# Optimization experiments

Hardware: AMD Instinct MI355X
Metric: run time of the kernel (lower is better)

The kernel has to match this reference:

```python
import jax, jax.numpy as jnp
import numpy as np

D_MODEL, D_K, D_V, H = 1024, 64, 64, 16
B, N = 4, 2048


def setup_inputs() -> dict:
    key = jax.random.key(0)
    ks = jax.random.split(key, 11)
    s = 0.02
    return {
        "Q": jax.random.normal(ks[0], (B, N, D_MODEL), jnp.float32),
        "K": jax.random.normal(ks[1], (B, N, D_MODEL), jnp.float32),
        "V": jax.random.normal(ks[2], (B, N, D_MODEL), jnp.float32),
        # stacked per-head projection weights: [h, d_model, d_k]
        "Wq": jax.random.normal(ks[3], (H, D_MODEL, D_K), jnp.float32) * s,
        "bq": jax.random.normal(ks[4], (H, D_K), jnp.float32) * s,
        "Wk": jax.random.normal(ks[5], (H, D_MODEL, D_K), jnp.float32) * s,
        "bk": jax.random.normal(ks[6], (H, D_K), jnp.float32) * s,
        "Wv": jax.random.normal(ks[7], (H, D_MODEL, D_V), jnp.float32) * s,
        "bv": jax.random.normal(ks[8], (H, D_V), jnp.float32) * s,
        "Wo": jax.random.normal(ks[9], (H * D_V, D_MODEL), jnp.float32) * s,
        "bo": jax.random.normal(ks[10], (D_MODEL,), jnp.float32) * s,
        "apply_mask": 1,
    }


def reference(Q, K, V, Wq, bq, Wk, bk, Wv, bv, Wo, bo, apply_mask):
    # fused per-head projections: [b, h, n, d_k]
    q = jnp.einsum("bnd,hdk->bhnk", Q, Wq) + bq[None, :, None, :]
    k = jnp.einsum("bnd,hdk->bhnk", K, Wk) + bk[None, :, None, :]
    v = jnp.einsum("bnd,hdv->bhnv", V, Wv) + bv[None, :, None, :]
    scores = jnp.einsum("bhnk,bhmk->bhnm", q, k) / jnp.sqrt(
        jnp.asarray(D_K, q.dtype)
    )
    if apply_mask:
        n = Q.shape[1]
        causal = jnp.tril(jnp.ones((n, n), dtype=bool))
        scores = jnp.where(causal[None, None], scores, -jnp.inf)
    weights = jax.nn.softmax(scores, axis=-1)
    out = jnp.einsum("bhnm,bhmv->bhnv", weights, v)
    # concat heads: [b, n, h*d_v]
    out = out.transpose(0, 2, 1, 3).reshape(Q.shape[0], Q.shape[1], H * D_V)
    return out @ Wo + bo
```

## Files before the change

### kernel.cpp

```cpp
#include <hip/hip_runtime.h>
#include <hip/hip_bf16.h>

#define H 16
#define DM 1024
#define DK 64
#define B_ 4
#define N_ 2048

typedef __attribute__((ext_vector_type(8))) short bf16x8;
typedef __attribute__((ext_vector_type(4))) short s16x4;
typedef __attribute__((ext_vector_type(4))) float f32x4;

static __device__ __forceinline__ short f2bs(float x) {
    __hip_bfloat16 b = __float2bfloat16(x);
    return *reinterpret_cast<short*>(&b);
}

static __device__ __forceinline__ void async16(const void* g, void* l) {
    __builtin_amdgcn_global_load_lds(
        (const __attribute__((address_space(1))) void*)g,
        (__attribute__((address_space(3))) void*)l, 16, 0, 0);
}

__global__ __launch_bounds__(256) void prep_kernel(
    const float* __restrict__ Q, const float* __restrict__ K, const float* __restrict__ V,
    const float* __restrict__ Wq, const float* __restrict__ Wk,
    const float* __restrict__ Wv, const float* __restrict__ Wo,
    short* __restrict__ Qb, short* __restrict__ Kb, short* __restrict__ Vb,
    short* __restrict__ wqT, short* __restrict__ wkT,
    short* __restrict__ wvT, short* __restrict__ woT)
{
    int y = blockIdx.y;
    if (y < 3) {
        const float* s = (y == 0) ? Q : (y == 1) ? K : V;
        short* d = (y == 0) ? Qb : (y == 1) ? Kb : Vb;
        size_t i = ((size_t)blockIdx.x * 256 + threadIdx.x) * 8;
        f32x4 a = *(const f32x4*)(s + i);
        f32x4 b = *(const f32x4*)(s + i + 4);
        bf16x8 p;
        #pragma unroll
        for (int j = 0; j < 4; ++j) { p[j] = f2bs(a[j]); p[4 + j] = f2bs(b[j]); }
        *(bf16x8*)(d + i) = p;
        return;
    }
    if (blockIdx.x >= 1024) return;
    __shared__ float tile[64][65];
    int z = blockIdx.x >> 8;
    int bx = blockIdx.x & 255;
    int t = threadIdx.x;
    int tj = t & 63, ti = t >> 6;

    if (z < 3) {
        const float* src = (z == 0) ? Wq : (z == 1) ? Wk : Wv;
        short* dst = (z == 0) ? wqT : (z == 1) ? wkT : wvT;
        int h = bx >> 4;
        int dmt = bx & 15;
        #pragma unroll
        for (int r = 0; r < 16; ++r) {
            int i = r * 4 + ti;
            tile[i][tj] = src[((size_t)h * 1024 + dmt * 64 + i) * 64 + tj];
        }
        __syncthreads();
        #pragma unroll
        for (int r = 0; r < 16; ++r) {
            int dk = r * 4 + ti;
            dst[((size_t)h * 64 + dk) * 1024 + dmt * 64 + tj] = f2bs(tile[tj][dk]);
        }
    } else {
        int kt = bx >> 4;
        int nt = bx & 15;
        #pragma unroll
        for (int r = 0; r < 16; ++r) {
            int i = r * 4 + ti;
            tile[i][tj] = Wo[((size_t)kt * 64 + i) * 1024 + nt * 64 + tj];
        }
        __syncthreads();
        #pragma unroll
        for (int r = 0; r < 16; ++r) {
            int jn = r * 4 + ti;
            woT[((size_t)nt * 64 + jn) * 1024 + kt * 64 + tj] = f2bs(tile[tj][jn]);
        }
    }
}

static __device__ __forceinline__ void gemm_stage(
    const char* Ab, const char* Bb, size_t kb, char* As, char* Bs, int lane, int w)
{
    int r0 = w * 32 + (lane >> 2);
    int g  = ((lane & 3) ^ ((lane >> 3) & 3)) << 4;
    int dst0 = w * 2048 + lane * 16;
    async16(Ab + (size_t)r0 * 2048 + kb + g, As + dst0);
    async16(Ab + (size_t)(r0 + 16) * 2048 + kb + g, As + dst0 + 1024);
    async16(Bb + (size_t)r0 * 2048 + kb + g, Bs + dst0);
    async16(Bb + (size_t)(r0 + 16) * 2048 + kb + g, Bs + dst0 + 1024);
}

static __device__ __forceinline__ void gemm_mainloop(
    const short* __restrict__ A, const short* __restrict__ BT,
    int rowM0, int colN0, char* As, char* Bs, f32x4 (&acc)[4][4])
{
    int tid = threadIdx.x;
    int lane = tid & 63, w = tid >> 6;
    int l16 = lane & 15, quad = lane >> 4;
    int wm = w >> 1, wn = w & 1;
    int xg = (quad ^ ((l16 >> 1) & 3)) << 4;

    const char* Ab = (const char*)A + (size_t)rowM0 * 2048;
    const char* Bb = (const char*)BT + (size_t)colN0 * 2048;

    gemm_stage(Ab, Bb, 0, As, Bs, lane, w);
    for (int it = 0; it < 32; ++it) {
        __syncthreads();
        int cur = (it & 1) * 8192;
        if (it + 1 < 32) {
            int nxt = ((it + 1) & 1) * 8192;
            gemm_stage(Ab, Bb, (size_t)(it + 1) * 64, As + nxt, Bs + nxt, lane, w);
        }
        bf16x8 a[4], b[4];
        #pragma unroll
        for (int i = 0; i < 4; ++i)
            a[i] = *(const bf16x8*)(As + cur + (wm * 64 + i * 16 + l16) * 64 + xg);
        #pragma unroll
        for (int j = 0; j < 4; ++j)
            b[j] = *(const bf16x8*)(Bs + cur + (wn * 64 + j * 16 + l16) * 64 + xg);
        #pragma unroll
        for (int i = 0; i < 4; ++i)
            #pragma unroll
            for (int j = 0; j < 4; ++j)
                acc[i][j] = __builtin_amdgcn_mfma_f32_16x16x32_bf16(a[i], b[j], acc[i][j], 0, 0, 0);
    }
}

__global__ __launch_bounds__(256) void proj_gemm(
    const short* __restrict__ Qb, const short* __restrict__ Kb, const short* __restrict__ Vb,
    const short* __restrict__ wqT, const short* __restrict__ wkT, const short* __restrict__ wvT,
    const float* __restrict__ bq, const float* __restrict__ bk, const float* __restrict__ bv,
    short* __restrict__ qbuf, short* __restrict__ kbuf, short* __restrict__ vTbuf)
{
    __shared__ char As[16384], Bs[16384];
    int which = blockIdx.z;
    const short* A  = (which == 0) ? Qb : (which == 1) ? Kb : Vb;
    const short* BT = (which == 0) ? wqT : (which == 1) ? wkT : wvT;
    const float* bias = (which == 0) ? bq : (which == 1) ? bk : bv;

    int rowM0 = blockIdx.x * 128;
    int colN0 = blockIdx.y * 128;

    f32x4 acc[4][4];
    #pragma unroll
    for (int i = 0; i < 4; ++i)
        #pragma unroll
        for (int j = 0; j < 4; ++j) acc[i][j] = (f32x4){0.f, 0.f, 0.f, 0.f};

    gemm_mainloop(A, BT, rowM0, colN0, As, Bs, acc);

    int lane = threadIdx.x & 63, w = threadIdx.x >> 6;
    int l16 = lane & 15, quad = lane >> 4;
    int wm = w >> 1, wn = w & 1;

    if (which == 2) {
        #pragma unroll
        for (int j = 0; j < 4; ++j) {
            int col = colN0 + wn * 64 + j * 16 + l16;
            int hh = col >> 6, dv = col & 63;
            float bs = bias[col];
            #pragma unroll
            for (int i = 0; i < 4; ++i) {
                int rowb = rowM0 + wm * 64 + i * 16 + quad * 4;
                int bb = rowb >> 11, n0 = rowb & 2047;
                s16x4 pk;
                #pragma unroll
                for (int r = 0; r < 4; ++r) pk[r] = f2bs(acc[i][j][r] + bs);
                *(s16x4*)(vTbuf + (((size_t)bb * H + hh) * DK + dv) * N_ + n0) = pk;
            }
        }
    } else {
        short* dst = (which == 0) ? qbuf : kbuf;
        float scl = (which == 0) ? 0.180336880f : 1.0f;
        #pragma unroll
        for (int j = 0; j < 4; ++j) {
            int col = colN0 + wn * 64 + j * 16 + l16;
            float bs = bias[col];
            #pragma unroll
            for (int i = 0; i < 4; ++i) {
                int rowb = rowM0 + wm * 64 + i * 16 + quad * 4;
                #pragma unroll
                for (int r = 0; r < 4; ++r)
                    dst[(size_t)(rowb + r) * 1024 + col] = f2bs((acc[i][j][r] + bs) * scl);
            }
        }
    }
}

__global__ __launch_bounds__(256) void out_gemm(
    const short* __restrict__ obuf, const short* __restrict__ woT,
    const float* __restrict__ bo, float* __restrict__ out)
{
    __shared__ char As[16384], Bs[16384];
    int rowM0 = blockIdx.x * 128;
    int colN0 = blockIdx.y * 128;

    f32x4 acc[4][4];
    #pragma unroll
    for (int i = 0; i < 4; ++i)
        #pragma unroll
        for (int j = 0; j < 4; ++j) acc[i][j] = (f32x4){0.f, 0.f, 0.f, 0.f};

    gemm_mainloop(obuf, woT, rowM0, colN0, As, Bs, acc);

    int lane = threadIdx.x & 63, w = threadIdx.x >> 6;
    int l16 = lane & 15, quad = lane >> 4;
    int wm = w >> 1, wn = w & 1;

    #pragma unroll
    for (int j = 0; j < 4; ++j) {
        int col = colN0 + wn * 64 + j * 16 + l16;
        float bs = bo[col];
        #pragma unroll
        for (int i = 0; i < 4; ++i) {
            int rowb = rowM0 + wm * 64 + i * 16 + quad * 4;
            #pragma unroll
            for (int r = 0; r < 4; ++r)
                out[(size_t)(rowb + r) * 1024 + col] = acc[i][j][r] + bs;
        }
    }
}

__global__ __launch_bounds__(256) void flash_kernel(
    const short* __restrict__ qbuf, const short* __restrict__ kbuf, const short* __restrict__ vT,
    short* __restrict__ obuf, const int* __restrict__ amask)
{
    __shared__ short Ks[2][4096];
    __shared__ short Vs[2][4096];
    __shared__ char  plds[4][2048];

    int bid = blockIdx.x;
    int g = bid & 7, idx = bid >> 3;
    int bh = g * 8 + (idx >> 4);
    int xq = idx & 15;
    int b = bh >> 4, h = bh & 15;

    int tid = threadIdx.x;
    int lane = tid & 63, wave = tid >> 6;
    int l16 = lane & 15, quad = lane >> 4;
    int msk = amask[0];

    int i8 = lane >> 3, i7 = lane & 7;
    int sg = (i7 ^ i8) << 4;
    int pk0 = i8 * 4 + wave;
    int skey = wave * 16 + i8;
    int ldst = wave * 2048 + lane * 16;

    const char* kbase = (const char*)(kbuf + (size_t)b * 2048 * 1024 + h * 64);
    const char* vbase = (const char*)(vT + ((size_t)(b * 16 + h) * 64) * 2048);

    int m7 = l16 & 7;
    int g0 = (quad ^ m7) << 4;
    int g1 = ((4 | quad) ^ m7) << 4;

    char* pw = plds[wave];
    int prd0 = l16 * 128 + g0;
    int prd1 = l16 * 128 + g1;

    for (int pass = 0; pass < 2; ++pass) {
        int qt = pass ? (31 - xq) : xq;
        int qw = qt * 64 + wave * 16;
        int nkb = msk ? (qt + 1) : 32;

        const short* qp = qbuf + ((size_t)(b * 2048 + qw + l16)) * 1024 + h * 64;
        bf16x8 aq0 = *(const bf16x8*)(qp + quad * 8);
        bf16x8 aq1 = *(const bf16x8*)(qp + 32 + quad * 8);

        f32x4 o[4];
        float lsum[4];
        #pragma unroll
        for (int i = 0; i < 4; ++i) { o[i] = (f32x4){0.f, 0.f, 0.f, 0.f}; lsum[i] = 0.f; }

        async16(kbase + (size_t)pk0 * 2048 + sg, (char*)Ks[0] + ldst);
        async16(kbase + (size_t)(pk0 + 32) * 2048 + sg, (char*)Ks[0] + ldst + 1024);
        async16(vbase + (size_t)skey * 4096 + sg, (char*)Vs[0] + ldst);
        async16(vbase + (size_t)(skey + 8) * 4096 + sg, (char*)Vs[0] + ldst + 1024);

        for (int ib = 0; ib < nkb; ++ib) {
            __syncthreads();
            int cur = ib & 1;
            if (ib + 1 < nkb) {
                int nb = (ib + 1) & 1;
                size_t kb2 = (size_t)(ib + 1) * 64;
                async16(kbase + (kb2 + pk0) * 2048 + sg, (char*)Ks[nb] + ldst);
                async16(kbase + (kb2 + pk0 + 32) * 2048 + sg, (char*)Ks[nb] + ldst + 1024);
                async16(vbase + (size_t)skey * 4096 + kb2 * 2 + sg, (char*)Vs[nb] + ldst);
                async16(vbase + (size_t)(skey + 8) * 4096 + kb2 * 2 + sg, (char*)Vs[nb] + ldst + 1024);
            }
            int kb = ib * 64;

            f32x4 s[4];
            #pragma unroll
            for (int nt = 0; nt < 4; ++nt) {
                const char* kr = (const char*)Ks[cur] + (nt * 16 + l16) * 128;
                bf16x8 b0 = *(const bf16x8*)(kr + g0);
                bf16x8 b1 = *(const bf16x8*)(kr + g1);
                f32x4 t = (f32x4){0.f, 0.f, 0.f, 0.f};
                t = __builtin_amdgcn_mfma_f32_16x16x32_bf16(aq0, b0, t, 0, 0, 0);
                t = __builtin_amdgcn_mfma_f32_16x16x32_bf16(aq1, b1, t, 0, 0, 0);
                s[nt] = t;
            }

            if (msk && (kb + 63 > qw)) {
                #pragma unroll
                for (int r = 0; r < 4; ++r) {
                    int row = qw + quad * 4 + r;
                    #pragma unroll
                    for (int nt = 0; nt < 4; ++nt) {
                        int col = kb + l16 * 4 + nt;
                        if (col > row) s[nt][r] = -3e38f;
                    }
                }
            }

            #pragma unroll
            for (int r = 0; r < 4; ++r) {
                float p0 = exp2f(s[0][r]), p1 = exp2f(s[1][r]);
                float p2 = exp2f(s[2][r]), p3 = exp2f(s[3][r]);
                s[0][r] = p0; s[1][r] = p1; s[2][r] = p2; s[3][r] = p3;
                lsum[r] += (p0 + p1) + (p2 + p3);
            }

            __builtin_amdgcn_wave_barrier();
            #pragma unroll
            for (int r = 0; r < 4; ++r) {
                int row = quad * 4 + r;
                s16x4 pk;
                pk[0] = f2bs(s[0][r]); pk[1] = f2bs(s[1][r]);
                pk[2] = f2bs(s[2][r]); pk[3] = f2bs(s[3][r]);
                *(s16x4*)(pw + row * 128 + (((l16 >> 1) ^ (row & 7)) << 4) + ((l16 & 1) << 3)) = pk;
            }
            __builtin_amdgcn_wave_barrier();
            bf16x8 ap0 = *(const bf16x8*)(pw + prd0);
            bf16x8 ap1 = *(const bf16x8*)(pw + prd1);
            __builtin_amdgcn_wave_barrier();

            #pragma unroll
            for (int vb = 0; vb < 4; ++vb) {
                const char* vr = (const char*)Vs[cur] + (vb * 16 + l16) * 128;
                bf16x8 v0 = *(const bf16x8*)(vr + g0);
                bf16x8 v1 = *(const bf16x8*)(vr + g1);
                o[vb] = __builtin_amdgcn_mfma_f32_16x16x32_bf16(ap0, v0, o[vb], 0, 0, 0);
                o[vb] = __builtin_amdgcn_mfma_f32_16x16x32_bf16(ap1, v1, o[vb], 0, 0, 0);
            }
        }

        #pragma unroll
        for (int r = 0; r < 4; ++r) {
            float t = lsum[r];
            #pragma unroll
            for (int off = 1; off < 16; off <<= 1) t += __shfl_xor(t, off, 64);
            float inv = 1.0f / t;
            int row = qw + quad * 4 + r;
            #pragma unroll
            for (int vb = 0; vb < 4; ++vb)
                obuf[((size_t)(b * 2048 + row)) * 1024 + h * 64 + vb * 16 + l16] =
                    f2bs(o[vb][r] * inv);
        }
        __syncthreads();
    }
}

extern "C" void kernel_launch(void* const* d_in, const int* in_sizes, int n_in,
                              void* d_out, int out_size, void* d_ws, size_t ws_size,
                              hipStream_t stream)
{
    const float* Q  = (const float*)d_in[0];
    const float* K  = (const float*)d_in[1];
    const float* V  = (const float*)d_in[2];
    const float* Wq = (const float*)d_in[3];
    const float* bq = (const float*)d_in[4];
    const float* Wk = (const float*)d_in[5];
    const float* bk = (const float*)d_in[6];
    const float* Wv = (const float*)d_in[7];
    const float* bv = (const float*)d_in[8];
    const float* Wo = (const float*)d_in[9];
    const float* bo = (const float*)d_in[10];
    const int* amask = (const int*)d_in[11];
    float* out = (float*)d_out;

    char* ws = (char*)d_ws;
    const size_t SZ = (size_t)B_ * N_ * DM * sizeof(short);
    const size_t SZW = (size_t)H * DK * DM * sizeof(short);
    short* Qb    = (short*)ws; ws += SZ;
    short* Kb    = (short*)ws; ws += SZ;
    short* Vb    = (short*)ws; ws += SZ;
    short* qbuf  = (short*)ws; ws += SZ;
    short* kbuf  = (short*)ws; ws += SZ;
    short* vTbuf = (short*)ws; ws += SZ;
    short* wqT   = (short*)ws; ws += SZW;
    short* wkT   = (short*)ws; ws += SZW;
    short* wvT   = (short*)ws; ws += SZW;
    short* woT   = (short*)ws; ws += SZW;
    short* obuf  = Qb;

    prep_kernel<<<dim3(4096, 4), dim3(256), 0, stream>>>(Q, K, V, Wq, Wk, Wv, Wo,
                                                         Qb, Kb, Vb, wqT, wkT, wvT, woT);
    proj_gemm<<<dim3(64, 8, 3), dim3(256), 0, stream>>>(Qb, Kb, Vb, wqT, wkT, wvT,
                                                        bq, bk, bv, qbuf, kbuf, vTbuf);
    flash_kernel<<<dim3(1024), dim3(256), 0, stream>>>(qbuf, kbuf, vTbuf, obuf, amask);
    out_gemm<<<dim3(64, 8), dim3(256), 0, stream>>>(obuf, woT, bo, out);
}
```

Before: 358.1 us.

## Use register-staged GEMM loads, raw exp2, and truncating bf16 pack in attention

The GEMM mainloop swaps async global-to-LDS double buffering for loads into registers that are then stored to a single LDS buffer, which halves shared memory per block and adds a second barrier per iteration. In the attention kernel, exp2f becomes the hardware exp2 builtin and the P values are packed to bf16 with a byte permute (truncation rather than round-to-nearest). Swizzled write addresses are precomputed once. The aim is higher occupancy and fewer VALU instructions in the softmax, at the cost of slightly lower precision and less load/compute overlap in the GEMM.

```diff
diff --git a/kernel.cpp b/kernel.cpp
--- a/kernel.cpp
+++ b/kernel.cpp
@@ -9,6 +9,7 @@
 
 typedef __attribute__((ext_vector_type(8))) short bf16x8;
 typedef __attribute__((ext_vector_type(4))) short s16x4;
+typedef __attribute__((ext_vector_type(2))) unsigned int u32x2;
 typedef __attribute__((ext_vector_type(4))) float f32x4;
 
 static __device__ __forceinline__ short f2bs(float x) {
@@ -20,6 +21,10 @@
     __builtin_amdgcn_global_load_lds(
         (const __attribute__((address_space(1))) void*)g,
         (__attribute__((address_space(3))) void*)l, 16, 0, 0);
+}
+
+static __device__ __forceinline__ unsigned packbf(float lo, float hi) {
+    return __builtin_amdgcn_perm(__float_as_uint(hi), __float_as_uint(lo), 0x07060302u);
 }
 
 __global__ __launch_bounds__(256) void prep_kernel(
@@ -83,18 +88,6 @@
     }
 }
 
-static __device__ __forceinline__ void gemm_stage(
-    const char* Ab, const char* Bb, size_t kb, char* As, char* Bs, int lane, int w)
-{
-    int r0 = w * 32 + (lane >> 2);
-    int g  = ((lane & 3) ^ ((lane >> 3) & 3)) << 4;
-    int dst0 = w * 2048 + lane * 16;
-    async16(Ab + (size_t)r0 * 2048 + kb + g, As + dst0);
-    async16(Ab + (size_t)(r0 + 16) * 2048 + kb + g, As + dst0 + 1024);
-    async16(Bb + (size_t)r0 * 2048 + kb + g, Bs + dst0);
-    async16(Bb + (size_t)(r0 + 16) * 2048 + kb + g, Bs + dst0 + 1024);
-}
-
 static __device__ __forceinline__ void gemm_mainloop(
     const short* __restrict__ A, const short* __restrict__ BT,
     int rowM0, int colN0, char* As, char* Bs, f32x4 (&acc)[4][4])
@@ -105,24 +98,41 @@
     int wm = w >> 1, wn = w & 1;
     int xg = (quad ^ ((l16 >> 1) & 3)) << 4;
 
-    const char* Ab = (const char*)A + (size_t)rowM0 * 2048;
-    const char* Bb = (const char*)BT + (size_t)colN0 * 2048;
-
-    gemm_stage(Ab, Bb, 0, As, Bs, lane, w);
+    int r0 = w * 32 + (lane >> 2);
+    int gsl = ((lane & 3) ^ ((lane >> 3) & 3)) << 4;
+    int dst0 = w * 2048 + lane * 16;
+    const char* Ag0 = (const char*)A + (size_t)(rowM0 + r0) * 2048 + gsl;
+    const char* Ag1 = (const char*)A + (size_t)(rowM0 + r0 + 16) * 2048 + gsl;
+    const char* Bg0 = (const char*)BT + (size_t)(colN0 + r0) * 2048 + gsl;
+    const char* Bg1 = (const char*)BT + (size_t)(colN0 + r0 + 16) * 2048 + gsl;
+
+    bf16x8 ga0 = *(const bf16x8*)Ag0;
+    bf16x8 ga1 = *(const bf16x8*)Ag1;
+    bf16x8 gb0 = *(const bf16x8*)Bg0;
+    bf16x8 gb1 = *(const bf16x8*)Bg1;
+
     for (int it = 0; it < 32; ++it) {
+        if (it) __syncthreads();
+        *(bf16x8*)(As + dst0) = ga0;
+        *(bf16x8*)(As + dst0 + 1024) = ga1;
+        *(bf16x8*)(Bs + dst0) = gb0;
+        *(bf16x8*)(Bs + dst0 + 1024) = gb1;
+        if (it + 1 < 32) {
+            size_t kb = (size_t)(it + 1) * 64;
+            ga0 = *(const bf16x8*)(Ag0 + kb);
+            ga1 = *(const bf16x8*)(Ag1 + kb);
+            gb0 = *(const bf16x8*)(Bg0 + kb);
+            gb1 = *(const bf16x8*)(Bg1 + kb);
+        }
         __syncthreads();
-        int cur = (it & 1) * 8192;
-        if (it + 1 < 32) {
-            int nxt = ((it + 1) & 1) * 8192;
-            gemm_stage(Ab, Bb, (size_t)(it + 1) * 64, As + nxt, Bs + nxt, lane, w);
-        }
+
         bf16x8 a[4], b[4];
         #pragma unroll
         for (int i = 0; i < 4; ++i)
-            a[i] = *(const bf16x8*)(As + cur + (wm * 64 + i * 16 + l16) * 64 + xg);
+            a[i] = *(const bf16x8*)(As + (wm * 64 + i * 16 + l16) * 64 + xg);
         #pragma unroll
         for (int j = 0; j < 4; ++j)
-            b[j] = *(const bf16x8*)(Bs + cur + (wn * 64 + j * 16 + l16) * 64 + xg);
+            b[j] = *(const bf16x8*)(Bs + (wn * 64 + j * 16 + l16) * 64 + xg);
         #pragma unroll
         for (int i = 0; i < 4; ++i)
             #pragma unroll
@@ -137,7 +147,7 @@
     const float* __restrict__ bq, const float* __restrict__ bk, const float* __restrict__ bv,
     short* __restrict__ qbuf, short* __restrict__ kbuf, short* __restrict__ vTbuf)
 {
-    __shared__ char As[16384], Bs[16384];
+    __shared__ char As[8192], Bs[8192];
     int which = blockIdx.z;
     const short* A  = (which == 0) ? Qb : (which == 1) ? Kb : Vb;
     const short* BT = (which == 0) ? wqT : (which == 1) ? wkT : wvT;
@@ -196,7 +206,7 @@
     const short* __restrict__ obuf, const short* __restrict__ woT,
     const float* __restrict__ bo, float* __restrict__ out)
 {
-    __shared__ char As[16384], Bs[16384];
+    __shared__ char As[8192], Bs[8192];
     int rowM0 = blockIdx.x * 128;
     int colN0 = blockIdx.y * 128;
 
@@ -261,6 +271,12 @@
     char* pw = plds[wave];
     int prd0 = l16 * 128 + g0;
     int prd1 = l16 * 128 + g1;
+    int pwa[4];
+    #pragma unroll
+    for (int r = 0; r < 4; ++r) {
+        int row = quad * 4 + r;
+        pwa[r] = row * 128 + (((l16 >> 1) ^ (row & 7)) << 4) + ((l16 & 1) << 3);
+    }
 
     for (int pass = 0; pass < 2; ++pass) {
         int qt = pass ? (31 - xq) : xq;
@@ -318,22 +334,18 @@
                 }
             }
 
+            __builtin_amdgcn_wave_barrier();
             #pragma unroll
             for (int r = 0; r < 4; ++r) {
-                float p0 = exp2f(s[0][r]), p1 = exp2f(s[1][r]);
-                float p2 = exp2f(s[2][r]), p3 = exp2f(s[3][r]);
-                s[0][r] = p0; s[1][r] = p1; s[2][r] = p2; s[3][r] = p3;
+                float p0 = __builtin_amdgcn_exp2f(s[0][r]);
+                float p1 = __builtin_amdgcn_exp2f(s[1][r]);
+                float p2 = __builtin_amdgcn_exp2f(s[2][r]);
+                float p3 = __builtin_amdgcn_exp2f(s[3][r]);
                 lsum[r] += (p0 + p1) + (p2 + p3);
-            }
-
-            __builtin_amdgcn_wave_barrier();
-            #pragma unroll
-            for (int r = 0; r < 4; ++r) {
-                int row = quad * 4 + r;
-                s16x4 pk;
-                pk[0] = f2bs(s[0][r]); pk[1] = f2bs(s[1][r]);
-                pk[2] = f2bs(s[2][r]); pk[3] = f2bs(s[3][r]);
-                *(s16x4*)(pw + row * 128 + (((l16 >> 1) ^ (row & 7)) << 4) + ((l16 & 1) << 3)) = pk;
+                u32x2 pk;
+                pk[0] = packbf(p0, p1);
+                pk[1] = packbf(p2, p3);
+                *(u32x2*)(pw + pwa[r]) = pk;
             }
             __builtin_amdgcn_wave_barrier();
             bf16x8 ap0 = *(const bf16x8*)(pw + prd0);
```

After: 325.3 us. 1.1x faster.
